# Kernel tuning notes

Hardware: AMD Instinct MI355X
Metric: run time of the kernel (lower is better)

The kernel has to match this reference:

```python
import jax, jax.numpy as jnp
import numpy as np

FEATURES = 4
HIDDEN = 32


def setup_inputs() -> dict:
    key = jax.random.key(0)
    ks = jax.random.split(key, 12)
    n_nodes, n_edges = 100000, 2500000
    x = jax.random.normal(ks[0], (n_nodes, FEATURES), dtype=jnp.float32)
    edge_index = jax.random.randint(ks[1], (2, n_edges), 0, n_nodes, dtype=jnp.int64)
    def glorot(k, fan_in, fan_out):
        s = jnp.sqrt(6.0 / (fan_in + fan_out)).astype(jnp.float32)
        return jax.random.uniform(k, (fan_in, fan_out), jnp.float32, -s, s)
    return {
        "x": x,
        "edge_index": edge_index,
        "W1": glorot(ks[2], FEATURES, HIDDEN), "b1": jnp.zeros((HIDDEN,), jnp.float32),
        "W2": glorot(ks[3], HIDDEN, HIDDEN),   "b2": jnp.zeros((HIDDEN,), jnp.float32),
        "W21": glorot(ks[4], HIDDEN, HIDDEN),  "b21": jnp.zeros((HIDDEN,), jnp.float32),
        "W3": glorot(ks[5], HIDDEN, 1),        "b3": jnp.zeros((1,), jnp.float32),
    }


def _gcn_norm(edge_index, n_nodes):
    # Add self-loops, compute symmetric normalization deg^-1/2[dst]*deg^-1/2[src]
    loops = jnp.arange(n_nodes, dtype=edge_index.dtype)
    src = jnp.concatenate([edge_index[0], loops])
    dst = jnp.concatenate([edge_index[1], loops])
    deg = jax.ops.segment_sum(jnp.ones_like(dst, dtype=jnp.float32), dst, num_segments=n_nodes)
    dinv = jnp.where(deg > 0, jax.lax.rsqrt(deg), 0.0)
    norm = dinv[src] * dinv[dst]  # [E+N]
    return src, dst, norm


def _gcn_layer(x, W, b, src, dst, norm, n_nodes):
    h = x @ W                                   # [N, out]
    msg = h[src] * norm[:, None]                # gather + scale
    out = jax.ops.segment_sum(msg, dst, num_segments=n_nodes)  # scatter-add
    return out + b


def reference(x, edge_index, W1, b1, W2, b2, W21, b21, W3, b3):
    n_nodes = x.shape[0]
    src, dst, norm = _gcn_norm(edge_index, n_nodes)
    h = jax.nn.relu(_gcn_layer(x, W1, b1, src, dst, norm, n_nodes))
    h = jax.nn.relu(_gcn_layer(h, W2, b2, src, dst, norm, n_nodes))
    h = jax.nn.relu(_gcn_layer(h, W21, b21, src, dst, norm, n_nodes))
    return _gcn_layer(h, W3, b3, src, dst, norm, n_nodes)
```

## Files before the change

### kernel.cpp

```cpp
#include <hip/hip_runtime.h>

#define FEATS 4
#define HID 32
#define BLK 256
#define CAP 64
#define PW 256
#define PSHIFT 8
#define PCAP 8192
#define NPB 512
#define PBLK 1024
#define MAXK 8
#define MAXNP 512

static inline int cdiv(long long a, int b) { return (int)((a + b - 1) / b); }

__global__ void k_zero_i(int* __restrict__ p, int n) {
    int i = blockIdx.x * blockDim.x + threadIdx.x;
    if (i < n) p[i] = 0;
}

__global__ void __launch_bounds__(PBLK, 4)
k_partition(const int* __restrict__ src, const int* __restrict__ dst,
            int* __restrict__ part_fill, unsigned int* __restrict__ part_edges,
            int e, int np) {
    __shared__ int lcnt[MAXNP];
    __shared__ int lbase[MAXNP];
    for (int p = threadIdx.x; p < np; p += blockDim.x) lcnt[p] = 0;
    __syncthreads();
    int chunk = (e + gridDim.x - 1) / gridDim.x;
    int lo = blockIdx.x * chunk;
    int hi = min(lo + chunk, e);
    unsigned pw[MAXK];
    int pp[MAXK];
#pragma unroll
    for (int k = 0; k < MAXK; k++) {
        int j = lo + threadIdx.x + k * (int)blockDim.x;
        if (j < hi) {
            int d = dst[j], s = src[j];
            int p = d >> PSHIFT;
            pp[k] = p;
            pw[k] = (unsigned)s | ((unsigned)(d & (PW - 1)) << 24);
            atomicAdd(&lcnt[p], 1);
        } else pp[k] = -1;
    }
    __syncthreads();
    for (int p = threadIdx.x; p < np; p += blockDim.x) {
        int c = lcnt[p];
        lbase[p] = c ? atomicAdd(&part_fill[p], c) : 0;
        lcnt[p] = 0;
    }
    __syncthreads();
#pragma unroll
    for (int k = 0; k < MAXK; k++) {
        if (pp[k] >= 0) {
            int p = pp[k];
            int pos = lbase[p] + atomicAdd(&lcnt[p], 1);
            if (pos < PCAP) part_edges[(size_t)p * PCAP + pos] = pw[k];
        }
    }
}

__global__ void k_local_csr(const int* __restrict__ part_fill,
                            const unsigned int* __restrict__ part_edges,
                            const float4* __restrict__ x,
                            int* __restrict__ cnt_g, float* __restrict__ dinv,
                            float4* __restrict__ xn, int* __restrict__ bucket, int n) {
    __shared__ int cnt[PW];
    int p = blockIdx.x;
    if (threadIdx.x < PW) cnt[threadIdx.x] = 0;
    __syncthreads();
    int m = min(part_fill[p], PCAP);
    const unsigned int* pe = part_edges + (size_t)p * PCAP;
    int base_node = p << PSHIFT;
    for (int j = threadIdx.x; j < m; j += blockDim.x) {
        unsigned v = pe[j];
        int local = (int)(v >> 24);
        int s = (int)(v & 0xFFFFFFu);
        int pos = atomicAdd(&cnt[local], 1);
        if (pos < CAP) bucket[(size_t)(base_node + local) * CAP + pos] = s;
    }
    __syncthreads();
    if (threadIdx.x < PW) {
        int node = base_node + threadIdx.x;
        if (node < n) {
            int dg = cnt[threadIdx.x];
            cnt_g[node] = dg;
            float s = rsqrtf((float)(dg + 1));
            dinv[node] = s;
            float4 v = x[node];
            v.x *= s; v.y *= s; v.z *= s; v.w *= s;
            xn[node] = v;
        }
    }
}

__global__ void k_dinv(const int* __restrict__ deg, float* __restrict__ dinv, int n) {
    int i = blockIdx.x * blockDim.x + threadIdx.x;
    if (i < n) dinv[i] = rsqrtf((float)(deg[i] + 1));
}

__global__ void k_gather4_f12(const int* __restrict__ cnt, const int* __restrict__ bucket,
                              const float4* __restrict__ xn, const float* __restrict__ dinv,
                              const float* __restrict__ W1, const float* __restrict__ b1,
                              const float* __restrict__ W2, float* __restrict__ hn, int n) {
    __shared__ float4 sW1[FEATS * 8];
    __shared__ float4 sB1[8];
    __shared__ float4 sW2[HID * 8];
    int tid = threadIdx.x;
    if (tid < FEATS * 8) sW1[tid] = ((const float4*)W1)[tid];
    if (tid < 8) sB1[tid] = ((const float4*)b1)[tid];
    sW2[tid] = ((const float4*)W2)[tid];
    __syncthreads();
    int gid = blockIdx.x * blockDim.x + tid;
    int node = gid >> 3;
    int cq = gid & 7;
    if (node >= n) return;
    int dg = min(cnt[node], CAP);
    const int* row = bucket + (size_t)node * CAP;
    float4 acc = make_float4(0.f, 0.f, 0.f, 0.f);
    int j = cq;
    for (; j + 8 < dg; j += 16) {
        int s0 = row[j], s1 = row[j + 8];
        float4 v0 = xn[s0];
        float4 v1 = xn[s1];
        acc.x += v0.x + v1.x; acc.y += v0.y + v1.y;
        acc.z += v0.z + v1.z; acc.w += v0.w + v1.w;
    }
    if (j < dg) {
        float4 v = xn[row[j]];
        acc.x += v.x; acc.y += v.y; acc.z += v.z; acc.w += v.w;
    }
#pragma unroll
    for (int m = 1; m < 8; m <<= 1) {
        acc.x += __shfl_xor(acc.x, m, 8);
        acc.y += __shfl_xor(acc.y, m, 8);
        acc.z += __shfl_xor(acc.z, m, 8);
        acc.w += __shfl_xor(acc.w, m, 8);
    }
    float sc = dinv[node];
    float4 self = xn[node];
    float4 a;
    a.x = sc * (acc.x + self.x);
    a.y = sc * (acc.y + self.y);
    a.z = sc * (acc.z + self.z);
    a.w = sc * (acc.w + self.w);
    float4 w0 = sW1[0 * 8 + cq], w1 = sW1[1 * 8 + cq];
    float4 w2 = sW1[2 * 8 + cq], w3 = sW1[3 * 8 + cq];
    float4 y = sB1[cq];
    y.x += a.x * w0.x + a.y * w1.x + a.z * w2.x + a.w * w3.x;
    y.y += a.x * w0.y + a.y * w1.y + a.z * w2.y + a.w * w3.y;
    y.z += a.x * w0.z + a.y * w1.z + a.z * w2.z + a.w * w3.z;
    y.w += a.x * w0.w + a.y * w1.w + a.z * w2.w + a.w * w3.w;
    y.x = fmaxf(y.x, 0.f); y.y = fmaxf(y.y, 0.f);
    y.z = fmaxf(y.z, 0.f); y.w = fmaxf(y.w, 0.f);
    float4 o = make_float4(0.f, 0.f, 0.f, 0.f);
#pragma unroll
    for (int r = 0; r < 8; r++) {
        float4 v;
        v.x = __shfl(y.x, r, 8);
        v.y = __shfl(y.y, r, 8);
        v.z = __shfl(y.z, r, 8);
        v.w = __shfl(y.w, r, 8);
        float4 wa = sW2[(4 * r + 0) * 8 + cq];
        float4 wb = sW2[(4 * r + 1) * 8 + cq];
        float4 wc = sW2[(4 * r + 2) * 8 + cq];
        float4 wd = sW2[(4 * r + 3) * 8 + cq];
        o.x += v.x * wa.x + v.y * wb.x + v.z * wc.x + v.w * wd.x;
        o.y += v.x * wa.y + v.y * wb.y + v.z * wc.y + v.w * wd.y;
        o.z += v.x * wa.z + v.y * wb.z + v.z * wc.z + v.w * wd.z;
        o.w += v.x * wa.w + v.y * wb.w + v.z * wc.w + v.w * wd.w;
    }
    o.x *= sc; o.y *= sc; o.z *= sc; o.w *= sc;
    ((float4*)hn)[node * 8 + cq] = o;
}

template <int K, int C>
__global__ void k_mm(const float* __restrict__ in, const float* __restrict__ W,
                     const float* __restrict__ dinv, float* __restrict__ hn, int n) {
    __shared__ float sW[K * C];
    for (int i = threadIdx.x; i < K * C; i += blockDim.x) sW[i] = W[i];
    __syncthreads();
    int gid = blockIdx.x * blockDim.x + threadIdx.x;
    int node = gid / C, c = gid % C;
    if (node >= n) return;
    float acc = 0.0f;
#pragma unroll
    for (int k = 0; k < K; k++) acc += in[node * K + k] * sW[k * C + c];
    hn[node * C + c] = acc * dinv[node];
}

#define ACC4(v) do { acc.x += (v).x; acc.y += (v).y; acc.z += (v).z; acc.w += (v).w; } while (0)

#define GATHER_BODY()                                                        \
    int dg = min(cnt[node], CAP);                                            \
    const float4* hp = (const float4*)hn;                                    \
    const int* row = bucket + (size_t)node * CAP;                            \
    float4 acc = hp[node * 8 + cq];                                          \
    int j = 0;                                                               \
    for (; j + 8 <= dg; j += 8) {                                            \
        int4 sa = *(const int4*)(row + j);                                   \
        int4 sb = *(const int4*)(row + j + 4);                               \
        float4 v0 = hp[sa.x * 8 + cq];                                       \
        float4 v1 = hp[sa.y * 8 + cq];                                       \
        float4 v2 = hp[sa.z * 8 + cq];                                       \
        float4 v3 = hp[sa.w * 8 + cq];                                       \
        float4 v4 = hp[sb.x * 8 + cq];                                       \
        float4 v5 = hp[sb.y * 8 + cq];                                       \
        float4 v6 = hp[sb.z * 8 + cq];                                       \
        float4 v7 = hp[sb.w * 8 + cq];                                       \
        ACC4(v0); ACC4(v1); ACC4(v2); ACC4(v3);                              \
        ACC4(v4); ACC4(v5); ACC4(v6); ACC4(v7);                              \
    }                                                                        \
    if (j + 4 <= dg) {                                                       \
        int4 s4 = *(const int4*)(row + j);                                   \
        float4 v0 = hp[s4.x * 8 + cq];                                       \
        float4 v1 = hp[s4.y * 8 + cq];                                       \
        float4 v2 = hp[s4.z * 8 + cq];                                       \
        float4 v3 = hp[s4.w * 8 + cq];                                       \
        ACC4(v0); ACC4(v1); ACC4(v2); ACC4(v3);                              \
        j += 4;                                                              \
    }                                                                        \
    for (; j < dg; j++) {                                                    \
        float4 v = hp[row[j] * 8 + cq];                                      \
        ACC4(v);                                                             \
    }

__global__ void k_gather_fmm(const int* __restrict__ cnt, const int* __restrict__ bucket,
                             const float* __restrict__ hn, const float* __restrict__ dinv,
                             const float* __restrict__ bias, const float* __restrict__ Wn,
                             float* __restrict__ hn3, int n) {
    __shared__ float4 sW[HID * 8];
    sW[threadIdx.x] = ((const float4*)Wn)[threadIdx.x];
    __syncthreads();
    int gid = blockIdx.x * blockDim.x + threadIdx.x;
    int node = gid >> 3;
    int cq = gid & 7;
    if (node >= n) return;
    GATHER_BODY()
    float sc = dinv[node];
    float4 b = ((const float4*)bias)[cq];
    float4 y;
    y.x = fmaxf(sc * acc.x + b.x, 0.f);
    y.y = fmaxf(sc * acc.y + b.y, 0.f);
    y.z = fmaxf(sc * acc.z + b.z, 0.f);
    y.w = fmaxf(sc * acc.w + b.w, 0.f);
    float4 o = make_float4(0.f, 0.f, 0.f, 0.f);
#pragma unroll
    for (int r = 0; r < 8; r++) {
        float4 v;
        v.x = __shfl(y.x, r, 8);
        v.y = __shfl(y.y, r, 8);
        v.z = __shfl(y.z, r, 8);
        v.w = __shfl(y.w, r, 8);
        float4 w0 = sW[(4 * r + 0) * 8 + cq];
        float4 w1 = sW[(4 * r + 1) * 8 + cq];
        float4 w2 = sW[(4 * r + 2) * 8 + cq];
        float4 w3 = sW[(4 * r + 3) * 8 + cq];
        o.x += v.x * w0.x + v.y * w1.x + v.z * w2.x + v.w * w3.x;
        o.y += v.x * w0.y + v.y * w1.y + v.z * w2.y + v.w * w3.y;
        o.z += v.x * w0.z + v.y * w1.z + v.z * w2.z + v.w * w3.z;
        o.w += v.x * w0.w + v.y * w1.w + v.z * w2.w + v.w * w3.w;
    }
    o.x *= sc; o.y *= sc; o.z *= sc; o.w *= sc;
    ((float4*)hn3)[node * 8 + cq] = o;
}

__global__ void k_gather_fdot(const int* __restrict__ cnt, const int* __restrict__ bucket,
                              const float* __restrict__ hn, const float* __restrict__ dinv,
                              const float* __restrict__ bias, const float* __restrict__ W3,
                              float* __restrict__ hn4, int n) {
    int gid = blockIdx.x * blockDim.x + threadIdx.x;
    int node = gid >> 3;
    int cq = gid & 7;
    if (node >= n) return;
    GATHER_BODY()
    float sc = dinv[node];
    float4 b = ((const float4*)bias)[cq];
    float4 w = ((const float4*)W3)[cq];
    float p = fmaxf(sc * acc.x + b.x, 0.f) * w.x
            + fmaxf(sc * acc.y + b.y, 0.f) * w.y
            + fmaxf(sc * acc.z + b.z, 0.f) * w.z
            + fmaxf(sc * acc.w + b.w, 0.f) * w.w;
#pragma unroll
    for (int o = 4; o > 0; o >>= 1) p += __shfl_down(p, o, 8);
    if (cq == 0) hn4[node] = p * sc;
}

__global__ void k_gather1b(const int* __restrict__ cnt, const int* __restrict__ bucket,
                           const float* __restrict__ hn, const float* __restrict__ dinv,
                           const float* __restrict__ b, float* __restrict__ out, int n) {
    int gid = blockIdx.x * blockDim.x + threadIdx.x;
    int node = gid >> 3;
    int lane = gid & 7;
    if (node >= n) return;
    int dg = min(cnt[node], CAP);
    const int* row = bucket + (size_t)node * CAP;
    float acc = (lane == 0) ? hn[node] : 0.0f;
    int j = lane;
    for (; j + 8 < dg; j += 16) {
        float a0 = hn[row[j]];
        float a1 = hn[row[j + 8]];
        acc += a0 + a1;
    }
    if (j < dg) acc += hn[row[j]];
#pragma unroll
    for (int o = 4; o > 0; o >>= 1) acc += __shfl_down(acc, o, 8);
    if (lane == 0) out[node] = dinv[node] * acc + b[0];
}

__global__ void k_deg_count(const int* __restrict__ dst, int* __restrict__ deg, int e) {
    int i = blockIdx.x * blockDim.x + threadIdx.x;
    if (i < e) atomicAdd(&deg[dst[i]], 1);
}

__global__ void k_block_scan(const int* __restrict__ deg, int* __restrict__ exc,
                             int* __restrict__ blk_sums, int n) {
    __shared__ int s[BLK];
    int i = blockIdx.x * BLK + threadIdx.x;
    int v = (i < n) ? deg[i] : 0;
    s[threadIdx.x] = v;
    __syncthreads();
    for (int off = 1; off < BLK; off <<= 1) {
        int t = (threadIdx.x >= (unsigned)off) ? s[threadIdx.x - off] : 0;
        __syncthreads();
        s[threadIdx.x] += t;
        __syncthreads();
    }
    if (i < n) exc[i] = s[threadIdx.x] - v;
    if (threadIdx.x == BLK - 1) blk_sums[blockIdx.x] = s[threadIdx.x];
}

__global__ void k_scan_sums(int* __restrict__ blk_sums, int nb) {
    __shared__ int s[1024];
    __shared__ int carry;
    if (threadIdx.x == 0) carry = 0;
    __syncthreads();
    for (int base = 0; base < nb; base += 1024) {
        int i = base + threadIdx.x;
        int v = (i < nb) ? blk_sums[i] : 0;
        s[threadIdx.x] = v;
        __syncthreads();
        for (int off = 1; off < 1024; off <<= 1) {
            int t = (threadIdx.x >= (unsigned)off) ? s[threadIdx.x - off] : 0;
            __syncthreads();
            s[threadIdx.x] += t;
            __syncthreads();
        }
        if (i < nb) blk_sums[i] = s[threadIdx.x] - v + carry;
        __syncthreads();
        if (threadIdx.x == 0) carry += s[1023];
        __syncthreads();
    }
}

__global__ void k_add_off(const int* __restrict__ exc, const int* __restrict__ blk_sums,
                          int* __restrict__ row_start, int* __restrict__ fill, int n) {
    int i = blockIdx.x * blockDim.x + threadIdx.x;
    if (i < n) {
        int rs = exc[i] + blk_sums[i / BLK];
        row_start[i] = rs;
        fill[i] = rs;
    }
}

__global__ void k_scatter(const int* __restrict__ src, const int* __restrict__ dst,
                          int* __restrict__ fill, int* __restrict__ csr_src, int e) {
    int i = blockIdx.x * blockDim.x + threadIdx.x;
    if (i < e) {
        int pos = atomicAdd(&fill[dst[i]], 1);
        csr_src[pos] = src[i];
    }
}

template <bool RELU>
__global__ void k_gather32(const int* __restrict__ row_start, const int* __restrict__ deg,
                           const int* __restrict__ csr_src, const float* __restrict__ hn,
                           const float* __restrict__ dinv, const float* __restrict__ bias,
                           float* __restrict__ y, int n) {
    int gid = blockIdx.x * blockDim.x + threadIdx.x;
    int node = gid >> 3;
    int cq = gid & 7;
    if (node >= n) return;
    int rs = row_start[node], dg = deg[node];
    const float4* hp = (const float4*)hn;
    float4 acc = hp[node * 8 + cq];
    for (int j = 0; j < dg; j++) {
        int s = csr_src[rs + j];
        float4 v = hp[s * 8 + cq];
        ACC4(v);
    }
    float sc = dinv[node];
    float4 b = ((const float4*)bias)[cq];
    float4 r;
    r.x = sc * acc.x + b.x; r.y = sc * acc.y + b.y;
    r.z = sc * acc.z + b.z; r.w = sc * acc.w + b.w;
    if (RELU) {
        r.x = fmaxf(r.x, 0.0f); r.y = fmaxf(r.y, 0.0f);
        r.z = fmaxf(r.z, 0.0f); r.w = fmaxf(r.w, 0.0f);
    }
    ((float4*)y)[node * 8 + cq] = r;
}

__global__ void k_gather1(const int* __restrict__ row_start, const int* __restrict__ deg,
                          const int* __restrict__ csr_src, const float* __restrict__ hn,
                          const float* __restrict__ dinv, const float* __restrict__ b,
                          float* __restrict__ out, int n) {
    int gid = blockIdx.x * blockDim.x + threadIdx.x;
    int node = gid >> 3;
    int lane = gid & 7;
    if (node >= n) return;
    int rs = row_start[node], dg = deg[node];
    float acc = (lane == 0) ? hn[node] : 0.0f;
    for (int j = lane; j < dg; j += 8) acc += hn[csr_src[rs + j]];
#pragma unroll
    for (int o = 4; o > 0; o >>= 1) acc += __shfl_down(acc, o, 8);
    if (lane == 0) out[node] = dinv[node] * acc + b[0];
}

extern "C" void kernel_launch(void* const* d_in, const int* in_sizes, int n_in,
                              void* d_out, int out_size, void* d_ws, size_t ws_size,
                              hipStream_t stream) {
    const float* x   = (const float*)d_in[0];
    const int*   ei  = (const int*)d_in[1];
    const float* W1  = (const float*)d_in[2];
    const float* b1  = (const float*)d_in[3];
    const float* W2  = (const float*)d_in[4];
    const float* b2  = (const float*)d_in[5];
    const float* W21 = (const float*)d_in[6];
    const float* b21 = (const float*)d_in[7];
    const float* W3  = (const float*)d_in[8];
    const float* b3  = (const float*)d_in[9];
    float* out = (float*)d_out;

    const int n = in_sizes[0] / FEATS;
    const int e = in_sizes[1] / 2;
    const int* src = ei;
    const int* dst = ei + e;
    const int nb = cdiv(n, BLK);
    const int np = cdiv(n, PW);

    auto align256 = [](size_t v) { return (v + 255) & ~(size_t)255; };
    const long long n8 = (long long)n * 8;

    size_t sz_cnt    = align256((size_t)n * 4);
    size_t sz_dinv   = align256((size_t)n * 4);
    size_t sz_f4     = align256((size_t)n * 16);
    size_t sz_bucket = align256((size_t)n * CAP * 4);
    size_t sz_hn     = align256((size_t)n * HID * 4);
    size_t sz_part   = align256((size_t)np * PCAP * 4) + align256((size_t)np * 4);
    size_t region    = 2 * sz_hn > sz_part ? 2 * sz_hn : sz_part;
    size_t need = sz_cnt + sz_dinv + sz_f4 + sz_bucket + region;

    if (ws_size >= need && np <= MAXNP && (long long)e <= (long long)NPB * PBLK * MAXK) {
        char* ws = (char*)d_ws;
        size_t off = 0;
        int*    cnt_g  = (int*)(ws + off);    off += sz_cnt;
        float*  dinv   = (float*)(ws + off);  off += sz_dinv;
        float4* xn     = (float4*)(ws + off); off += sz_f4;
        int*    bucket = (int*)(ws + off);    off += sz_bucket;
        char*   reg    = ws + off;
        float* hn = (float*)reg;
        float* yb = (float*)(reg + sz_hn);
        unsigned int* part_edges = (unsigned int*)reg;
        int* part_fill = (int*)(reg + align256((size_t)np * PCAP * 4));

        k_zero_i<<<cdiv(np, BLK), BLK, 0, stream>>>(part_fill, np);
        k_partition<<<NPB, PBLK, 0, stream>>>(src, dst, part_fill, part_edges, e, np);
        k_local_csr<<<np, PBLK, 0, stream>>>(part_fill, part_edges, (const float4*)x,
                                             cnt_g, dinv, xn, bucket, n);

        k_gather4_f12<<<cdiv(n8, BLK), BLK, 0, stream>>>(cnt_g, bucket, xn, dinv,
                                                         W1, b1, W2, hn, n);

        k_gather_fmm<<<cdiv(n8, BLK), BLK, 0, stream>>>(cnt_g, bucket, hn, dinv, b2, W21, yb, n);
        k_gather_fdot<<<cdiv(n8, BLK), BLK, 0, stream>>>(cnt_g, bucket, yb, dinv, b21, W3, hn, n);
        k_gather1b<<<cdiv(n8, BLK), BLK, 0, stream>>>(cnt_g, bucket, hn, dinv, b3, out, n);
    } else {
        const long long nc = (long long)n * HID;
        char* ws = (char*)d_ws;
        size_t off = 0;
        int*   deg_i     = (int*)(ws + off);   off += align256((size_t)n * 4);
        int*   exc       = (int*)(ws + off);   off += align256((size_t)n * 4);
        int*   row_start = (int*)(ws + off);   off += align256((size_t)n * 4);
        int*   fill      = (int*)(ws + off);   off += align256((size_t)n * 4);
        int*   blk_sums  = (int*)(ws + off);   off += align256((size_t)nb * 4);
        float* dinv      = (float*)(ws + off); off += align256((size_t)n * 4);
        int*   csr_src   = (int*)(ws + off);   off += align256((size_t)e * 4);
        float* hn        = (float*)(ws + off); off += align256((size_t)n * HID * 4);
        float* yb        = (float*)(ws + off); off += align256((size_t)n * HID * 4);

        k_zero_i<<<nb, BLK, 0, stream>>>(deg_i, n);
        k_deg_count<<<cdiv(e, BLK), BLK, 0, stream>>>(dst, deg_i, e);
        k_dinv<<<nb, BLK, 0, stream>>>(deg_i, dinv, n);
        k_block_scan<<<nb, BLK, 0, stream>>>(deg_i, exc, blk_sums, n);
        k_scan_sums<<<1, 1024, 0, stream>>>(blk_sums, nb);
        k_add_off<<<nb, BLK, 0, stream>>>(exc, blk_sums, row_start, fill, n);
        k_scatter<<<cdiv(e, BLK), BLK, 0, stream>>>(src, dst, fill, csr_src, e);

        k_mm<FEATS, HID><<<cdiv(nc, BLK), BLK, 0, stream>>>(x, W1, dinv, hn, n);
        k_gather32<true><<<cdiv(n8, BLK), BLK, 0, stream>>>(row_start, deg_i, csr_src, hn, dinv, b1, yb, n);

        k_mm<HID, HID><<<cdiv(nc, BLK), BLK, 0, stream>>>(yb, W2, dinv, hn, n);
        k_gather32<true><<<cdiv(n8, BLK), BLK, 0, stream>>>(row_start, deg_i, csr_src, hn, dinv, b2, yb, n);

        k_mm<HID, HID><<<cdiv(nc, BLK), BLK, 0, stream>>>(yb, W21, dinv, hn, n);
        k_gather32<true><<<cdiv(n8, BLK), BLK, 0, stream>>>(row_start, deg_i, csr_src, hn, dinv, b21, yb, n);

        k_mm<HID, 1><<<cdiv(n, BLK), BLK, 0, stream>>>(yb, W3, dinv, hn, n);
        k_gather1<<<cdiv(n8, BLK), BLK, 0, stream>>>(row_start, deg_i, csr_src, hn, dinv, b3, out, n);
    }
}
```

Baseline: 246.4 us.

## Store hidden features as fp16 split into two column planes per gather pass

```diff
diff --git a/kernel.cpp b/kernel.cpp
--- a/kernel.cpp
+++ b/kernel.cpp
@@ -1,4 +1,5 @@
 #include <hip/hip_runtime.h>
+#include <hip/hip_fp16.h>
 
 #define FEATS 4
 #define HID 32
@@ -14,6 +15,10 @@
 
 static inline int cdiv(long long a, int b) { return (int)((a + b - 1) / b); }
 
+struct __align__(8) half4v { __half2 a, b; };
+
+typedef int vint4 __attribute__((ext_vector_type(4)));
+
 __global__ void k_zero_i(int* __restrict__ p, int n) {
     int i = blockIdx.x * blockDim.x + threadIdx.x;
     if (i < n) p[i] = 0;
@@ -102,7 +107,8 @@
 __global__ void k_gather4_f12(const int* __restrict__ cnt, const int* __restrict__ bucket,
                               const float4* __restrict__ xn, const float* __restrict__ dinv,
                               const float* __restrict__ W1, const float* __restrict__ b1,
-                              const float* __restrict__ W2, float* __restrict__ hn, int n) {
+                              const float* __restrict__ W2,
+                              __half* __restrict__ hA, __half* __restrict__ hB, int n) {
     __shared__ float4 sW1[FEATS * 8];
     __shared__ float4 sB1[8];
     __shared__ float4 sW2[HID * 8];
@@ -120,14 +126,15 @@
     float4 acc = make_float4(0.f, 0.f, 0.f, 0.f);
     int j = cq;
     for (; j + 8 < dg; j += 16) {
-        int s0 = row[j], s1 = row[j + 8];
+        int s0 = __builtin_nontemporal_load(row + j);
+        int s1 = __builtin_nontemporal_load(row + j + 8);
         float4 v0 = xn[s0];
         float4 v1 = xn[s1];
         acc.x += v0.x + v1.x; acc.y += v0.y + v1.y;
         acc.z += v0.z + v1.z; acc.w += v0.w + v1.w;
     }
     if (j < dg) {
-        float4 v = xn[row[j]];
+        float4 v = xn[__builtin_nontemporal_load(row + j)];
         acc.x += v.x; acc.y += v.y; acc.z += v.z; acc.w += v.w;
     }
 #pragma unroll
@@ -171,7 +178,12 @@
         o.w += v.x * wa.w + v.y * wb.w + v.z * wc.w + v.w * wd.w;
     }
     o.x *= sc; o.y *= sc; o.z *= sc; o.w *= sc;
-    ((float4*)hn)[node * 8 + cq] = o;
+    half4v st;
+    st.a = __floats2half2_rn(o.x, o.y);
+    st.b = __floats2half2_rn(o.z, o.w);
+    unsigned long long u = *(const unsigned long long*)&st;
+    __half* plane = (cq < 4) ? hA : hB;
+    __builtin_nontemporal_store(u, (unsigned long long*)plane + (size_t)node * 4 + (cq & 3));
 }
 
 template <int K, int C>
@@ -191,44 +203,60 @@
 
 #define ACC4(v) do { acc.x += (v).x; acc.y += (v).y; acc.z += (v).z; acc.w += (v).w; } while (0)
 
-#define GATHER_BODY()                                                        \
+#define ACCH2(v) do { float2 f_ = __half22float2(v); acc.x += f_.x; acc.y += f_.y; } while (0)
+
+#define GATHER_BODY_P(PLANE)                                                 \
     int dg = min(cnt[node], CAP);                                            \
-    const float4* hp = (const float4*)hn;                                    \
+    const __half2* hp = (const __half2*)(PLANE);                             \
     const int* row = bucket + (size_t)node * CAP;                            \
-    float4 acc = hp[node * 8 + cq];                                          \
+    float2 acc = __half22float2(hp[node * 8 + cq]);                          \
     int j = 0;                                                               \
     for (; j + 8 <= dg; j += 8) {                                            \
-        int4 sa = *(const int4*)(row + j);                                   \
-        int4 sb = *(const int4*)(row + j + 4);                               \
-        float4 v0 = hp[sa.x * 8 + cq];                                       \
-        float4 v1 = hp[sa.y * 8 + cq];                                       \
-        float4 v2 = hp[sa.z * 8 + cq];                                       \
-        float4 v3 = hp[sa.w * 8 + cq];                                       \
-        float4 v4 = hp[sb.x * 8 + cq];                                       \
-        float4 v5 = hp[sb.y * 8 + cq];                                       \
-        float4 v6 = hp[sb.z * 8 + cq];                                       \
-        float4 v7 = hp[sb.w * 8 + cq];                                       \
-        ACC4(v0); ACC4(v1); ACC4(v2); ACC4(v3);                              \
-        ACC4(v4); ACC4(v5); ACC4(v6); ACC4(v7);                              \
+        vint4 sa = __builtin_nontemporal_load((const vint4*)(row + j));      \
+        vint4 sb = __builtin_nontemporal_load((const vint4*)(row + j + 4));  \
+        __half2 v0 = hp[sa.x * 8 + cq];                                      \
+        __half2 v1 = hp[sa.y * 8 + cq];                                      \
+        __half2 v2 = hp[sa.z * 8 + cq];                                      \
+        __half2 v3 = hp[sa.w * 8 + cq];                                      \
+        __half2 v4 = hp[sb.x * 8 + cq];                                      \
+        __half2 v5 = hp[sb.y * 8 + cq];                                      \
+        __half2 v6 = hp[sb.z * 8 + cq];                                      \
+        __half2 v7 = hp[sb.w * 8 + cq];                                      \
+        ACCH2(v0); ACCH2(v1); ACCH2(v2); ACCH2(v3);                          \
+        ACCH2(v4); ACCH2(v5); ACCH2(v6); ACCH2(v7);                          \
     }                                                                        \
     if (j + 4 <= dg) {                                                       \
-        int4 s4 = *(const int4*)(row + j);                                   \
-        float4 v0 = hp[s4.x * 8 + cq];                                       \
-        float4 v1 = hp[s4.y * 8 + cq];                                       \
-        float4 v2 = hp[s4.z * 8 + cq];                                       \
-        float4 v3 = hp[s4.w * 8 + cq];                                       \
-        ACC4(v0); ACC4(v1); ACC4(v2); ACC4(v3);                              \
+        vint4 s4 = __builtin_nontemporal_load((const vint4*)(row + j));      \
+        __half2 v0 = hp[s4.x * 8 + cq];                                      \
+        __half2 v1 = hp[s4.y * 8 + cq];                                      \
+        __half2 v2 = hp[s4.z * 8 + cq];                                      \
+        __half2 v3 = hp[s4.w * 8 + cq];                                      \
+        ACCH2(v0); ACCH2(v1); ACCH2(v2); ACCH2(v3);                          \
         j += 4;                                                              \
     }                                                                        \
-    for (; j < dg; j++) {                                                    \
-        float4 v = hp[row[j] * 8 + cq];                                      \
-        ACC4(v);                                                             \
-    }
-
-__global__ void k_gather_fmm(const int* __restrict__ cnt, const int* __restrict__ bucket,
-                             const float* __restrict__ hn, const float* __restrict__ dinv,
-                             const float* __restrict__ bias, const float* __restrict__ Wn,
-                             float* __restrict__ hn3, int n) {
+    for (; j < dg; j++) { ACCH2(hp[row[j] * 8 + cq]); }
+
+__global__ void k_gfmmA(const int* __restrict__ cnt, const int* __restrict__ bucket,
+                        const __half* __restrict__ hA, const float* __restrict__ dinv,
+                        const float* __restrict__ bias, __half* __restrict__ yA, int n) {
+    int gid = blockIdx.x * blockDim.x + threadIdx.x;
+    int node = gid >> 3;
+    int cq = gid & 7;
+    if (node >= n) return;
+    GATHER_BODY_P(hA)
+    float sc = dinv[node];
+    float2 b = ((const float2*)bias)[cq];
+    __half2 st = __floats2half2_rn(fmaxf(sc * acc.x + b.x, 0.f),
+                                   fmaxf(sc * acc.y + b.y, 0.f));
+    unsigned u = *(const unsigned*)&st;
+    __builtin_nontemporal_store(u, (unsigned*)yA + (size_t)node * 8 + cq);
+}
+
+__global__ void k_gfmmB(const int* __restrict__ cnt, const int* __restrict__ bucket,
+                        const __half* __restrict__ hB, const float* __restrict__ dinv,
+                        const float* __restrict__ bias, const float* __restrict__ Wn,
+                        const __half* __restrict__ yA,
+                        __half* __restrict__ oA, __half* __restrict__ oB, int n) {
     __shared__ float4 sW[HID * 8];
     sW[threadIdx.x] = ((const float4*)Wn)[threadIdx.x];
     __syncthreads();
@@ -236,54 +264,74 @@
     int node = gid >> 3;
     int cq = gid & 7;
     if (node >= n) return;
-    GATHER_BODY()
+    GATHER_BODY_P(hB)
     float sc = dinv[node];
-    float4 b = ((const float4*)bias)[cq];
-    float4 y;
-    y.x = fmaxf(sc * acc.x + b.x, 0.f);
-    y.y = fmaxf(sc * acc.y + b.y, 0.f);
-    y.z = fmaxf(sc * acc.z + b.z, 0.f);
-    y.w = fmaxf(sc * acc.w + b.w, 0.f);
+    float2 b = ((const float2*)bias)[8 + cq];
+    float ybx = fmaxf(sc * acc.x + b.x, 0.f);
+    float yby = fmaxf(sc * acc.y + b.y, 0.f);
+    unsigned uy = __builtin_nontemporal_load((const unsigned*)yA + (size_t)node * 8 + cq);
+    float2 ya = __half22float2(*(const __half2*)&uy);
     float4 o = make_float4(0.f, 0.f, 0.f, 0.f);
 #pragma unroll
     for (int r = 0; r < 8; r++) {
-        float4 v;
-        v.x = __shfl(y.x, r, 8);
-        v.y = __shfl(y.y, r, 8);
-        v.z = __shfl(y.z, r, 8);
-        v.w = __shfl(y.w, r, 8);
-        float4 w0 = sW[(4 * r + 0) * 8 + cq];
-        float4 w1 = sW[(4 * r + 1) * 8 + cq];
-        float4 w2 = sW[(4 * r + 2) * 8 + cq];
-        float4 w3 = sW[(4 * r + 3) * 8 + cq];
-        o.x += v.x * w0.x + v.y * w1.x + v.z * w2.x + v.w * w3.x;
-        o.y += v.x * w0.y + v.y * w1.y + v.z * w2.y + v.w * w3.y;
-        o.z += v.x * w0.z + v.y * w1.z + v.z * w2.z + v.w * w3.z;
-        o.w += v.x * w0.w + v.y * w1.w + v.z * w2.w + v.w * w3.w;
+        float a0 = __shfl(ya.x, r, 8);
+        float a1 = __shfl(ya.y, r, 8);
+        float c0 = __shfl(ybx, r, 8);
+        float c1 = __shfl(yby, r, 8);
+        float4 w0 = sW[(2 * r + 0) * 8 + cq];
+        float4 w1 = sW[(2 * r + 1) * 8 + cq];
+        float4 w2 = sW[(16 + 2 * r) * 8 + cq];
+        float4 w3 = sW[(17 + 2 * r) * 8 + cq];
+        o.x += a0 * w0.x + a1 * w1.x + c0 * w2.x + c1 * w3.x;
+        o.y += a0 * w0.y + a1 * w1.y + c0 * w2.y + c1 * w3.y;
+        o.z += a0 * w0.z + a1 * w1.z + c0 * w2.z + c1 * w3.z;
+        o.w += a0 * w0.w + a1 * w1.w + c0 * w2.w + c1 * w3.w;
     }
     o.x *= sc; o.y *= sc; o.z *= sc; o.w *= sc;
-    ((float4*)hn3)[node * 8 + cq] = o;
-}
-
-__global__ void k_gather_fdot(const int* __restrict__ cnt, const int* __restrict__ bucket,
-                              const float* __restrict__ hn, const float* __restrict__ dinv,
-                              const float* __restrict__ bias, const float* __restrict__ W3,
-                              float* __restrict__ hn4, int n) {
+    half4v st;
+    st.a = __floats2half2_rn(o.x, o.y);
+    st.b = __floats2half2_rn(o.z, o.w);
+    unsigned long long u = *(const unsigned long long*)&st;
+    __half* plane = (cq < 4) ? oA : oB;
+    __builtin_nontemporal_store(u, (unsigned long long*)plane + (size_t)node * 4 + (cq & 3));
+}
+
+__global__ void k_gfdotA(const int* __restrict__ cnt, const int* __restrict__ bucket,
+                         const __half* __restrict__ hA, const float* __restrict__ dinv,
+                         const float* __restrict__ bias, const float* __restrict__ W3,
+                         float* __restrict__ pA, int n) {
     int gid = blockIdx.x * blockDim.x + threadIdx.x;
     int node = gid >> 3;
     int cq = gid & 7;
     if (node >= n) return;
-    GATHER_BODY()
+    GATHER_BODY_P(hA)
     float sc = dinv[node];
-    float4 b = ((const float4*)bias)[cq];
-    float4 w = ((const float4*)W3)[cq];
+    float2 b = ((const float2*)bias)[cq];
+    float2 w = ((const float2*)W3)[cq];
     float p = fmaxf(sc * acc.x + b.x, 0.f) * w.x
-            + fmaxf(sc * acc.y + b.y, 0.f) * w.y
-            + fmaxf(sc * acc.z + b.z, 0.f) * w.z
-            + fmaxf(sc * acc.w + b.w, 0.f) * w.w;
+            + fmaxf(sc * acc.y + b.y, 0.f) * w.y;
 #pragma unroll
     for (int o = 4; o > 0; o >>= 1) p += __shfl_down(p, o, 8);
-    if (cq == 0) hn4[node] = p * sc;
+    if (cq == 0) pA[node] = p;
+}
+
+__global__ void k_gfdotB(const int* __restrict__ cnt, const int* __restrict__ bucket,
+                         const __half* __restrict__ hB, const float* __restrict__ dinv,
+                         const float* __restrict__ bias, const float* __restrict__ W3,
+                         const float* __restrict__ pA, float* __restrict__ hn4, int n) {
+    int gid = blockIdx.x * blockDim.x + threadIdx.x;
+    int node = gid >> 3;
+    int cq = gid & 7;
+    if (node >= n) return;
+    GATHER_BODY_P(hB)
+    float sc = dinv[node];
+    float2 b = ((const float2*)bias)[8 + cq];
+    float2 w = ((const float2*)W3)[8 + cq];
+    float p = fmaxf(sc * acc.x + b.x, 0.f) * w.x
+            + fmaxf(sc * acc.y + b.y, 0.f) * w.y;
+#pragma unroll
+    for (int o = 4; o > 0; o >>= 1) p += __shfl_down(p, o, 8);
+    if (cq == 0) hn4[node] = (p + pA[node]) * sc;
 }
 
 __global__ void k_gather1b(const int* __restrict__ cnt, const int* __restrict__ bucket,
@@ -298,11 +346,11 @@
     float acc = (lane == 0) ? hn[node] : 0.0f;
     int j = lane;
     for (; j + 8 < dg; j += 16) {
-        float a0 = hn[row[j]];
-        float a1 = hn[row[j + 8]];
+        float a0 = hn[__builtin_nontemporal_load(row + j)];
+        float a1 = hn[__builtin_nontemporal_load(row + j + 8)];
         acc += a0 + a1;
     }
-    if (j < dg) acc += hn[row[j]];
+    if (j < dg) acc += hn[__builtin_nontemporal_load(row + j)];
 #pragma unroll
     for (int o = 4; o > 0; o >>= 1) acc += __shfl_down(acc, o, 8);
     if (lane == 0) out[node] = dinv[node] * acc + b[0];
@@ -446,9 +494,11 @@
     size_t sz_dinv   = align256((size_t)n * 4);
     size_t sz_f4     = align256((size_t)n * 16);
     size_t sz_bucket = align256((size_t)n * CAP * 4);
-    size_t sz_hn     = align256((size_t)n * HID * 4);
+    size_t P         = align256((size_t)n * 32);
+    size_t S         = align256((size_t)n * 4);
+    size_t sz_planes = 5 * P + 2 * S;
     size_t sz_part   = align256((size_t)np * PCAP * 4) + align256((size_t)np * 4);
-    size_t region    = 2 * sz_hn > sz_part ? 2 * sz_hn : sz_part;
+    size_t region    = sz_planes > sz_part ? sz_planes : sz_part;
     size_t need = sz_cnt + sz_dinv + sz_f4 + sz_bucket + region;
 
     if (ws_size >= need && np <= MAXNP && (long long)e <= (long long)NPB * PBLK * MAXK) {
@@ -459,8 +509,13 @@
         float4* xn     = (float4*)(ws + off); off += sz_f4;
         int*    bucket = (int*)(ws + off);    off += sz_bucket;
         char*   reg    = ws + off;
-        float* hn = (float*)reg;
-        float* yb = (float*)(reg + sz_hn);
+        __half* hA0 = (__half*)reg;
+        __half* hB0 = (__half*)(reg + P);
+        __half* hA1 = (__half*)(reg + 2 * P);
+        __half* hB1 = (__half*)(reg + 3 * P);
+        __half* yA  = (__half*)(reg + 4 * P);
+        float*  pA  = (float*)(reg + 5 * P);
+        float*  hn4 = (float*)(reg + 5 * P + S);
         unsigned int* part_edges = (unsigned int*)reg;
         int* part_fill = (int*)(reg + align256((size_t)np * PCAP * 4));
 
@@ -470,11 +525,17 @@
                                              cnt_g, dinv, xn, bucket, n);
 
         k_gather4_f12<<<cdiv(n8, BLK), BLK, 0, stream>>>(cnt_g, bucket, xn, dinv,
-                                                         W1, b1, W2, hn, n);
-
-        k_gather_fmm<<<cdiv(n8, BLK), BLK, 0, stream>>>(cnt_g, bucket, hn, dinv, b2, W21, yb, n);
-        k_gather_fdot<<<cdiv(n8, BLK), BLK, 0, stream>>>(cnt_g, bucket, yb, dinv, b21, W3, hn, n);
-        k_gather1b<<<cdiv(n8, BLK), BLK, 0, stream>>>(cnt_g, bucket, hn, dinv, b3, out, n);
+                                                         W1, b1, W2, hA0, hB0, n);
+
+        k_gfmmA<<<cdiv(n8, BLK), BLK, 0, stream>>>(cnt_g, bucket, hA0, dinv, b2, yA, n);
+        k_gfmmB<<<cdiv(n8, BLK), BLK, 0, stream>>>(cnt_g, bucket, hB0, dinv, b2, W21,
+                                                   yA, hA1, hB1, n);
+
+        k_gfdotA<<<cdiv(n8, BLK), BLK, 0, stream>>>(cnt_g, bucket, hA1, dinv, b21, W3, pA, n);
+        k_gfdotB<<<cdiv(n8, BLK), BLK, 0, stream>>>(cnt_g, bucket, hB1, dinv, b21, W3,
+                                                    pA, hn4, n);
+
+        k_gather1b<<<cdiv(n8, BLK), BLK, 0, stream>>>(cnt_g, bucket, hn4, dinv, b3, out, n);
     } else {
         const long long nc = (long long)n * HID;
         char* ws = (char*)d_ws;
```

After: 286.6 us. 16.3% more time.

## Store hidden features as fp16 and gather with 4 lanes per node

Applied to the files above, without the earlier changes.

```diff
diff --git a/kernel.cpp b/kernel.cpp
--- a/kernel.cpp
+++ b/kernel.cpp
@@ -1,4 +1,5 @@
 #include <hip/hip_runtime.h>
+#include <hip/hip_fp16.h>
 
 #define FEATS 4
 #define HID 32
@@ -14,6 +15,11 @@
 
 static inline int cdiv(long long a, int b) { return (int)((a + b - 1) / b); }
 
+struct __align__(8)  half4v { __half2 a, b; };
+struct __align__(16) half8v { __half2 a, b, c, d; };
+
+typedef int vint4 __attribute__((ext_vector_type(4)));
+
 __global__ void k_zero_i(int* __restrict__ p, int n) {
     int i = blockIdx.x * blockDim.x + threadIdx.x;
     if (i < n) p[i] = 0;
@@ -120,14 +126,15 @@
     float4 acc = make_float4(0.f, 0.f, 0.f, 0.f);
     int j = cq;
     for (; j + 8 < dg; j += 16) {
-        int s0 = row[j], s1 = row[j + 8];
+        int s0 = __builtin_nontemporal_load(row + j);
+        int s1 = __builtin_nontemporal_load(row + j + 8);
         float4 v0 = xn[s0];
         float4 v1 = xn[s1];
         acc.x += v0.x + v1.x; acc.y += v0.y + v1.y;
         acc.z += v0.z + v1.z; acc.w += v0.w + v1.w;
     }
     if (j < dg) {
-        float4 v = xn[row[j]];
+        float4 v = xn[__builtin_nontemporal_load(row + j)];
         acc.x += v.x; acc.y += v.y; acc.z += v.z; acc.w += v.w;
     }
 #pragma unroll
@@ -171,7 +178,10 @@
         o.w += v.x * wa.w + v.y * wb.w + v.z * wc.w + v.w * wd.w;
     }
     o.x *= sc; o.y *= sc; o.z *= sc; o.w *= sc;
-    ((float4*)hn)[node * 8 + cq] = o;
+    half4v st;
+    st.a = __floats2half2_rn(o.x, o.y);
+    st.b = __floats2half2_rn(o.z, o.w);
+    ((half4v*)hn)[node * 8 + cq] = st;
 }
 
 template <int K, int C>
@@ -191,78 +201,103 @@
 
 #define ACC4(v) do { acc.x += (v).x; acc.y += (v).y; acc.z += (v).z; acc.w += (v).w; } while (0)
 
-#define GATHER_BODY()                                                        \
+#define ACC8(v) do {                                                         \
+        float2 f0_ = __half22float2((v).a);                                  \
+        float2 f1_ = __half22float2((v).b);                                  \
+        float2 f2_ = __half22float2((v).c);                                  \
+        float2 f3_ = __half22float2((v).d);                                  \
+        acc0.x += f0_.x; acc0.y += f0_.y; acc0.z += f1_.x; acc0.w += f1_.y;  \
+        acc1.x += f2_.x; acc1.y += f2_.y; acc1.z += f3_.x; acc1.w += f3_.y;  \
+    } while (0)
+
+#define GATHER_BODY_H8()                                                     \
     int dg = min(cnt[node], CAP);                                            \
-    const float4* hp = (const float4*)hn;                                    \
+    const half8v* hp = (const half8v*)hn;                                    \
     const int* row = bucket + (size_t)node * CAP;                            \
-    float4 acc = hp[node * 8 + cq];                                          \
+    float4 acc0, acc1;                                                       \
+    {                                                                        \
+        half8v s_ = hp[node * 4 + q];                                        \
+        float2 f0_ = __half22float2(s_.a), f1_ = __half22float2(s_.b);       \
+        float2 f2_ = __half22float2(s_.c), f3_ = __half22float2(s_.d);       \
+        acc0 = make_float4(f0_.x, f0_.y, f1_.x, f1_.y);                      \
+        acc1 = make_float4(f2_.x, f2_.y, f3_.x, f3_.y);                      \
+    }                                                                        \
     int j = 0;                                                               \
     for (; j + 8 <= dg; j += 8) {                                            \
-        int4 sa = *(const int4*)(row + j);                                   \
-        int4 sb = *(const int4*)(row + j + 4);                               \
-        float4 v0 = hp[sa.x * 8 + cq];                                       \
-        float4 v1 = hp[sa.y * 8 + cq];                                       \
-        float4 v2 = hp[sa.z * 8 + cq];                                       \
-        float4 v3 = hp[sa.w * 8 + cq];                                       \
-        float4 v4 = hp[sb.x * 8 + cq];                                       \
-        float4 v5 = hp[sb.y * 8 + cq];                                       \
-        float4 v6 = hp[sb.z * 8 + cq];                                       \
-        float4 v7 = hp[sb.w * 8 + cq];                                       \
-        ACC4(v0); ACC4(v1); ACC4(v2); ACC4(v3);                              \
-        ACC4(v4); ACC4(v5); ACC4(v6); ACC4(v7);                              \
+        vint4 sa = __builtin_nontemporal_load((const vint4*)(row + j));      \
+        vint4 sb = __builtin_nontemporal_load((const vint4*)(row + j + 4));  \
+        half8v v0 = hp[sa.x * 4 + q];                                        \
+        half8v v1 = hp[sa.y * 4 + q];                                        \
+        half8v v2 = hp[sa.z * 4 + q];                                        \
+        half8v v3 = hp[sa.w * 4 + q];                                        \
+        half8v v4 = hp[sb.x * 4 + q];                                        \
+        half8v v5 = hp[sb.y * 4 + q];                                        \
+        half8v v6 = hp[sb.z * 4 + q];                                        \
+        half8v v7 = hp[sb.w * 4 + q];                                        \
+        ACC8(v0); ACC8(v1); ACC8(v2); ACC8(v3);                              \
+        ACC8(v4); ACC8(v5); ACC8(v6); ACC8(v7);                              \
     }                                                                        \
     if (j + 4 <= dg) {                                                       \
-        int4 s4 = *(const int4*)(row + j);                                   \
-        float4 v0 = hp[s4.x * 8 + cq];                                       \
-        float4 v1 = hp[s4.y * 8 + cq];                                       \
-        float4 v2 = hp[s4.z * 8 + cq];                                       \
-        float4 v3 = hp[s4.w * 8 + cq];                                       \
-        ACC4(v0); ACC4(v1); ACC4(v2); ACC4(v3);                              \
+        vint4 s4 = __builtin_nontemporal_load((const vint4*)(row + j));      \
+        half8v v0 = hp[s4.x * 4 + q];                                        \
+        half8v v1 = hp[s4.y * 4 + q];                                        \
+        half8v v2 = hp[s4.z * 4 + q];                                        \
+        half8v v3 = hp[s4.w * 4 + q];                                        \
+        ACC8(v0); ACC8(v1); ACC8(v2); ACC8(v3);                              \
         j += 4;                                                              \
     }                                                                        \
-    for (; j < dg; j++) {                                                    \
-        float4 v = hp[row[j] * 8 + cq];                                      \
-        ACC4(v);                                                             \
-    }
+    for (; j < dg; j++) { half8v v_ = hp[row[j] * 4 + q]; ACC8(v_); }
+
+#define YSEL(r) ((r) == 0 ? y0.x : (r) == 1 ? y0.y : (r) == 2 ? y0.z : \
+                 (r) == 3 ? y0.w : (r) == 4 ? y1.x : (r) == 5 ? y1.y : \
+                 (r) == 6 ? y1.z : y1.w)
 
 __global__ void k_gather_fmm(const int* __restrict__ cnt, const int* __restrict__ bucket,
                              const float* __restrict__ hn, const float* __restrict__ dinv,
                              const float* __restrict__ bias, const float* __restrict__ Wn,
                              float* __restrict__ hn3, int n) {
-    __shared__ float4 sW[HID * 8];
-    sW[threadIdx.x] = ((const float4*)Wn)[threadIdx.x];
-    __syncthreads();
-    int gid = blockIdx.x * blockDim.x + threadIdx.x;
-    int node = gid >> 3;
-    int cq = gid & 7;
-    if (node >= n) return;
-    GATHER_BODY()
+    __shared__ float4 sWa[HID * 4];
+    __shared__ float4 sWb[HID * 4];
+    int tid = threadIdx.x;
+    {
+        float4 f = ((const float4*)Wn)[tid];
+        int r = tid >> 3, c4 = tid & 7;
+        if (c4 & 1) sWb[r * 4 + (c4 >> 1)] = f;
+        else        sWa[r * 4 + (c4 >> 1)] = f;
+    }
+    __syncthreads();
+    int gid = blockIdx.x * blockDim.x + tid;
+    int node = gid >> 2;
+    int q = gid & 3;
+    if (node >= n) return;
+    GATHER_BODY_H8()
     float sc = dinv[node];
-    float4 b = ((const float4*)bias)[cq];
-    float4 y;
-    y.x = fmaxf(sc * acc.x + b.x, 0.f);
-    y.y = fmaxf(sc * acc.y + b.y, 0.f);
-    y.z = fmaxf(sc * acc.z + b.z, 0.f);
-    y.w = fmaxf(sc * acc.w + b.w, 0.f);
-    float4 o = make_float4(0.f, 0.f, 0.f, 0.f);
-#pragma unroll
-    for (int r = 0; r < 8; r++) {
-        float4 v;
-        v.x = __shfl(y.x, r, 8);
-        v.y = __shfl(y.y, r, 8);
-        v.z = __shfl(y.z, r, 8);
-        v.w = __shfl(y.w, r, 8);
-        float4 w0 = sW[(4 * r + 0) * 8 + cq];
-        float4 w1 = sW[(4 * r + 1) * 8 + cq];
-        float4 w2 = sW[(4 * r + 2) * 8 + cq];
-        float4 w3 = sW[(4 * r + 3) * 8 + cq];
-        o.x += v.x * w0.x + v.y * w1.x + v.z * w2.x + v.w * w3.x;
-        o.y += v.x * w0.y + v.y * w1.y + v.z * w2.y + v.w * w3.y;
-        o.z += v.x * w0.z + v.y * w1.z + v.z * w2.z + v.w * w3.z;
-        o.w += v.x * w0.w + v.y * w1.w + v.z * w2.w + v.w * w3.w;
-    }
-    o.x *= sc; o.y *= sc; o.z *= sc; o.w *= sc;
-    ((float4*)hn3)[node * 8 + cq] = o;
+    float4 b0 = ((const float4*)bias)[2 * q];
+    float4 b1 = ((const float4*)bias)[2 * q + 1];
+    float4 y0, y1;
+    y0.x = fmaxf(sc * acc0.x + b0.x, 0.f); y0.y = fmaxf(sc * acc0.y + b0.y, 0.f);
+    y0.z = fmaxf(sc * acc0.z + b0.z, 0.f); y0.w = fmaxf(sc * acc0.w + b0.w, 0.f);
+    y1.x = fmaxf(sc * acc1.x + b1.x, 0.f); y1.y = fmaxf(sc * acc1.y + b1.y, 0.f);
+    y1.z = fmaxf(sc * acc1.z + b1.z, 0.f); y1.w = fmaxf(sc * acc1.w + b1.w, 0.f);
+    float4 o0 = make_float4(0.f, 0.f, 0.f, 0.f);
+    float4 o1 = make_float4(0.f, 0.f, 0.f, 0.f);
+#pragma unroll
+    for (int r = 0; r < HID; r++) {
+        float yl = YSEL(r & 7);
+        float yr = __shfl(yl, r >> 3, 4);
+        float4 wa = sWa[r * 4 + q];
+        float4 wb = sWb[r * 4 + q];
+        o0.x += yr * wa.x; o0.y += yr * wa.y; o0.z += yr * wa.z; o0.w += yr * wa.w;
+        o1.x += yr * wb.x; o1.y += yr * wb.y; o1.z += yr * wb.z; o1.w += yr * wb.w;
+    }
+    o0.x *= sc; o0.y *= sc; o0.z *= sc; o0.w *= sc;
+    o1.x *= sc; o1.y *= sc; o1.z *= sc; o1.w *= sc;
+    half8v st;
+    st.a = __floats2half2_rn(o0.x, o0.y);
+    st.b = __floats2half2_rn(o0.z, o0.w);
+    st.c = __floats2half2_rn(o1.x, o1.y);
+    st.d = __floats2half2_rn(o1.z, o1.w);
+    ((half8v*)hn3)[node * 4 + q] = st;
 }
 
 __global__ void k_gather_fdot(const int* __restrict__ cnt, const int* __restrict__ bucket,
@@ -270,20 +305,26 @@
                               const float* __restrict__ bias, const float* __restrict__ W3,
                               float* __restrict__ hn4, int n) {
     int gid = blockIdx.x * blockDim.x + threadIdx.x;
-    int node = gid >> 3;
-    int cq = gid & 7;
-    if (node >= n) return;
-    GATHER_BODY()
+    int node = gid >> 2;
+    int q = gid & 3;
+    if (node >= n) return;
+    GATHER_BODY_H8()
     float sc = dinv[node];
-    float4 b = ((const float4*)bias)[cq];
-    float4 w = ((const float4*)W3)[cq];
-    float p = fmaxf(sc * acc.x + b.x, 0.f) * w.x
-            + fmaxf(sc * acc.y + b.y, 0.f) * w.y
-            + fmaxf(sc * acc.z + b.z, 0.f) * w.z
-            + fmaxf(sc * acc.w + b.w, 0.f) * w.w;
-#pragma unroll
-    for (int o = 4; o > 0; o >>= 1) p += __shfl_down(p, o, 8);
-    if (cq == 0) hn4[node] = p * sc;
+    float4 b0 = ((const float4*)bias)[2 * q];
+    float4 b1 = ((const float4*)bias)[2 * q + 1];
+    float4 w0 = ((const float4*)W3)[2 * q];
+    float4 w1 = ((const float4*)W3)[2 * q + 1];
+    float p = fmaxf(sc * acc0.x + b0.x, 0.f) * w0.x
+            + fmaxf(sc * acc0.y + b0.y, 0.f) * w0.y
+            + fmaxf(sc * acc0.z + b0.z, 0.f) * w0.z
+            + fmaxf(sc * acc0.w + b0.w, 0.f) * w0.w
+            + fmaxf(sc * acc1.x + b1.x, 0.f) * w1.x
+            + fmaxf(sc * acc1.y + b1.y, 0.f) * w1.y
+            + fmaxf(sc * acc1.z + b1.z, 0.f) * w1.z
+            + fmaxf(sc * acc1.w + b1.w, 0.f) * w1.w;
+    p += __shfl_down(p, 2, 4);
+    p += __shfl_down(p, 1, 4);
+    if (q == 0) hn4[node] = p * sc;
 }
 
 __global__ void k_gather1b(const int* __restrict__ cnt, const int* __restrict__ bucket,
@@ -298,11 +339,11 @@
     float acc = (lane == 0) ? hn[node] : 0.0f;
     int j = lane;
     for (; j + 8 < dg; j += 16) {
-        float a0 = hn[row[j]];
-        float a1 = hn[row[j + 8]];
+        float a0 = hn[__builtin_nontemporal_load(row + j)];
+        float a1 = hn[__builtin_nontemporal_load(row + j + 8)];
         acc += a0 + a1;
     }
-    if (j < dg) acc += hn[row[j]];
+    if (j < dg) acc += hn[__builtin_nontemporal_load(row + j)];
 #pragma unroll
     for (int o = 4; o > 0; o >>= 1) acc += __shfl_down(acc, o, 8);
     if (lane == 0) out[node] = dinv[node] * acc + b[0];
@@ -441,6 +482,7 @@
 
     auto align256 = [](size_t v) { return (v + 255) & ~(size_t)255; };
     const long long n8 = (long long)n * 8;
+    const long long n4 = (long long)n * 4;
 
     size_t sz_cnt    = align256((size_t)n * 4);
     size_t sz_dinv   = align256((size_t)n * 4);
@@ -472,8 +514,8 @@
         k_gather4_f12<<<cdiv(n8, BLK), BLK, 0, stream>>>(cnt_g, bucket, xn, dinv,
                                                          W1, b1, W2, hn, n);
 
-        k_gather_fmm<<<cdiv(n8, BLK), BLK, 0, stream>>>(cnt_g, bucket, hn, dinv, b2, W21, yb, n);
-        k_gather_fdot<<<cdiv(n8, BLK), BLK, 0, stream>>>(cnt_g, bucket, yb, dinv, b21, W3, hn, n);
+        k_gather_fmm<<<cdiv(n4, BLK), BLK, 0, stream>>>(cnt_g, bucket, hn, dinv, b2, W21, yb, n);
+        k_gather_fdot<<<cdiv(n4, BLK), BLK, 0, stream>>>(cnt_g, bucket, yb, dinv, b21, W3, hn, n);
         k_gather1b<<<cdiv(n8, BLK), BLK, 0, stream>>>(cnt_g, bucket, hn, dinv, b3, out, n);
     } else {
         const long long nc = (long long)n * HID;
```

After: 240.7 us. -2.3%, faster.
